# Optimization experiments

Measured on AMD Instinct MI355X. Metric: run time of the kernel, lower is better.

Reference implementation:

```python
import jax, jax.numpy as jnp
import numpy as np

SURROGATE_ALPHA = 2.0  # ATan surrogate sharpness (spikingjelly-style default)

@jax.custom_vjp
def spike_fn(x):
    return jnp.where(x > 0, 1.0, 0.0)

def _spike_fwd(x):
    return spike_fn(x), x

def _spike_bwd(x, g):
    # ATan surrogate gradient: alpha/2 / (1 + (pi/2 * alpha * x)^2)
    sg = SURROGATE_ALPHA / 2.0 / (1.0 + (jnp.pi / 2.0 * SURROGATE_ALPHA * x) ** 2)
    return (g * sg,)

spike_fn.defvjp(_spike_fwd, _spike_bwd)

def setup_inputs() -> dict:
    key = jax.random.key(0)
    B, N, T, D = 4, 1024, 128, 128  # [batch, nodes, time, feat]
    x = jax.random.normal(key, (B, N, T, D), dtype=jnp.float32)
    decay = jnp.zeros((D,), jnp.float32)  # nn.initializers.constant(0.0)
    v_th = jnp.zeros((D,), jnp.float32)   # nn.initializers.constant(0.0)
    return {"x": x, "decay": decay, "v_th": v_th}

def reference(x, decay, v_th):
    # time axis is dim 2 in the original module
    x_seq = jnp.moveaxis(x, 2, 0)  # [T, B, N, D]
    d = jax.nn.sigmoid(decay)          # per-feature learnable decay in (0,1)
    th = jax.nn.sigmoid(v_th) + 0.1    # per-feature learnable threshold > 0.1

    def scan_fn(v, x_t):
        v = v * d + x_t                        # leaky integrate
        s = spike_fn(v - th)                   # fire
        v = v * (1.0 - jax.lax.stop_gradient(s))  # hard reset (detached)
        return v, s

    v_init = jnp.zeros_like(x_seq[0])
    _, spikes = jax.lax.scan(scan_fn, v_init, x_seq)
    return jnp.moveaxis(spikes, 0, 2)  # back to [B, N, T, D]
```

## Files before the change

kernel.cpp:

```cpp
#include <hip/hip_runtime.h>
#include <math.h>


#define T_STEPS 128
#define D_FEAT  128

__global__ __launch_bounds__(256)
void plif_fwd_kernel(const float* __restrict__ x,
                     const float* __restrict__ decay,
                     const float* __restrict__ vth,
                     float* __restrict__ out)
{
    const int tid = blockIdx.x * blockDim.x + threadIdx.x;
    const int d   = tid & (D_FEAT - 1);
    const int row = tid >> 7;

    const size_t base = (size_t)row * (size_t)T_STEPS * D_FEAT + (size_t)d;
    const float* __restrict__ xr  = x + base;
    float* __restrict__       orw = out + base;

    const float dec = 1.0f / (1.0f + expf(-decay[d]));
    const float th  = 1.0f / (1.0f + expf(-vth[d])) + 0.1f;

    float v = 0.0f;

#pragma unroll 16
    for (int t = 0; t < T_STEPS; ++t) {
        const float xv = __builtin_nontemporal_load(xr + (size_t)t * D_FEAT);

        v = __fadd_rn(__fmul_rn(v, dec), xv);
        const bool f = (v > th);
        const float s = f ? 1.0f : 0.0f;
        v = f ? 0.0f : v;

        __builtin_nontemporal_store(s, orw + (size_t)t * D_FEAT);
    }
}

extern "C" void kernel_launch(void* const* d_in, const int* in_sizes, int n_in,
                              void* d_out, int out_size, void* d_ws, size_t ws_size,
                              hipStream_t stream)
{
    const float* x     = (const float*)d_in[0];
    const float* decay = (const float*)d_in[1];
    const float* vth   = (const float*)d_in[2];
    float*       out   = (float*)d_out;

    const int total   = in_sizes[0];
    const int rows    = total / (T_STEPS * D_FEAT);
    const int threads = rows * D_FEAT;
    const int block   = 256;

    plif_fwd_kernel<<<threads / block, block, 0, stream>>>(
        x, decay, vth, out);
}
```

Baseline: 102.5 us.

## Stage time chunks through shared memory with 128-bit vector loads and stores

Result: faster. 94.36 us (-8.0%).

```diff
diff --git a/kernel.cpp b/kernel.cpp
--- a/kernel.cpp
+++ b/kernel.cpp
@@ -4,36 +4,59 @@
 
 #define T_STEPS 128
 #define D_FEAT  128
+#define CT      8
+#define NCHUNK  (T_STEPS / CT)
+
+typedef float f32x4 __attribute__((ext_vector_type(4)));
 
 __global__ __launch_bounds__(256)
-void plif_fwd_kernel(const float* __restrict__ x,
+void plif_fwd_kernel(const f32x4* __restrict__ x4,
                      const float* __restrict__ decay,
                      const float* __restrict__ vth,
-                     float* __restrict__ out)
+                     f32x4* __restrict__ out4)
 {
-    const int tid = blockIdx.x * blockDim.x + threadIdx.x;
-    const int d   = tid & (D_FEAT - 1);
-    const int row = tid >> 7;
+    __shared__ float xs[2 * CT * D_FEAT];
+    __shared__ float ss[2 * CT * D_FEAT];
 
-    const size_t base = (size_t)row * (size_t)T_STEPS * D_FEAT + (size_t)d;
-    const float* __restrict__ xr  = x + base;
-    float* __restrict__       orw = out + base;
+    const int tid  = threadIdx.x;
+    const int lrow = tid >> 7;
+    const int d    = tid & (D_FEAT - 1);
+    const int r0   = blockIdx.x * 2;
 
     const float dec = 1.0f / (1.0f + expf(-decay[d]));
     const float th  = 1.0f / (1.0f + expf(-vth[d])) + 0.1f;
 
+    const size_t rowq = (size_t)T_STEPS * D_FEAT / 4;
+
     float v = 0.0f;
 
-#pragma unroll 16
-    for (int t = 0; t < T_STEPS; ++t) {
-        const float xv = __builtin_nontemporal_load(xr + (size_t)t * D_FEAT);
+    for (int c = 0; c < NCHUNK; ++c) {
+        const size_t cq = (size_t)(c * CT) * D_FEAT / 4;
 
-        v = __fadd_rn(__fmul_rn(v, dec), xv);
-        const bool f = (v > th);
-        const float s = f ? 1.0f : 0.0f;
-        v = f ? 0.0f : v;
+#pragma unroll
+        for (int p = 0; p < 2; ++p) {
+            const f32x4 tmp = __builtin_nontemporal_load(
+                x4 + (size_t)(r0 + p) * rowq + cq + (size_t)tid);
+            *(f32x4*)&xs[p * (CT * D_FEAT) + tid * 4] = tmp;
+        }
+        __syncthreads();
 
-        __builtin_nontemporal_store(s, orw + (size_t)t * D_FEAT);
+#pragma unroll
+        for (int i = 0; i < CT; ++i) {
+            const float xv = xs[lrow * (CT * D_FEAT) + i * D_FEAT + d];
+            v = __fadd_rn(__fmul_rn(v, dec), xv);
+            const bool f = (v > th);
+            ss[lrow * (CT * D_FEAT) + i * D_FEAT + d] = f ? 1.0f : 0.0f;
+            v = f ? 0.0f : v;
+        }
+        __syncthreads();
+
+#pragma unroll
+        for (int p = 0; p < 2; ++p) {
+            const f32x4 sv = *(const f32x4*)&ss[p * (CT * D_FEAT) + tid * 4];
+            __builtin_nontemporal_store(sv,
+                out4 + (size_t)(r0 + p) * rowq + cq + (size_t)tid);
+        }
     }
 }
 
@@ -46,11 +69,11 @@
     const float* vth   = (const float*)d_in[2];
     float*       out   = (float*)d_out;
 
-    const int total   = in_sizes[0];
-    const int rows    = total / (T_STEPS * D_FEAT);
-    const int threads = rows * D_FEAT;
-    const int block   = 256;
+    const int total  = in_sizes[0];
+    const int rows   = total / (T_STEPS * D_FEAT);
+    const int blocks = rows / 2;
+    const int block  = 256;
 
-    plif_fwd_kernel<<<threads / block, block, 0, stream>>>(
-        x, decay, vth, out);
+    plif_fwd_kernel<<<blocks, block, 0, stream>>>(
+        (const f32x4*)x, decay, vth, (f32x4*)out);
 }
```
